# Kernel optimization log

Hardware: AMD Instinct MI355X
Metric: run time of the kernel (lower is better)

## Reference

```python
import jax, jax.numpy as jnp
import numpy as np

# ---- fixed structuring elements (buffers, not trainable) ----
N_SCALES = 4
BASE = 2.0
ZERO_SCALE = 1.0
PAD_VAL = 10000.0

_scales = ZERO_SCALE ** 2 * np.power(BASE, np.arange(N_SCALES)) ** 2  # t_k = 4^k
_widths = [4 * int(np.ceil(np.sqrt(s))) for s in _scales]             # 4,8,16,32
SES = [jnp.asarray([(1.0 / (4.0 * t)) * x ** 2 for x in range(-w, w + 1)],
                   dtype=jnp.float32)
       for t, w in zip(_scales, _widths)]  # SE lengths 9,17,33,65 (all odd)


def _pool1d(im, se, c, axis, is_max):
    """Weighted sliding max/min along `axis` (separable morphological op).
    out[p] = max_j padded[p+j] - c*se[j]  (dilation) or min_j padded[p+j] + c*se[j]."""
    n = se.shape[0]
    w = n // 2  # n is odd -> symmetric pad, matches torch pad1==pad2
    pad_val = -PAD_VAL if is_max else PAD_VAL
    cfg = [(0, 0)] * im.ndim
    cfg[axis] = (w, w)
    padded = jnp.pad(im, cfg, constant_values=pad_val)
    L = im.shape[axis]

    def take(j):
        return jax.lax.dynamic_slice_in_dim(padded, j, L, axis)

    win = jax.vmap(take)(jnp.arange(n))          # [n, B, C, H, W]
    se_b = se.reshape((n,) + (1,) * im.ndim)     # broadcast over image dims
    if is_max:
        return jnp.max(win - c * se_b, axis=0)
    return jnp.min(win + c * se_b, axis=0)


def _sep_dilation(im, se, c):
    tmp = _pool1d(im, se, c, axis=-1, is_max=True)   # horizontal
    return _pool1d(tmp, se, c, axis=-2, is_max=True)  # vertical


def _sep_erosion(im, se, c):
    tmp = _pool1d(im, se, c, axis=-1, is_max=False)
    return _pool1d(tmp, se, c, axis=-2, is_max=False)


def setup_inputs() -> dict:
    key = jax.random.key(0)
    k1, _ = jax.random.split(key)
    inputs = jax.random.normal(k1, (4, 8, 256, 256), dtype=jnp.float32)
    se_coef = jnp.float32(0.5)
    return {"inputs": inputs, "se_coef": se_coef}


def reference(inputs, se_coef):
    # closing = erosion(dilation(x)) per scale, stacked on new axis 2
    outs = [_sep_erosion(_sep_dilation(inputs, se, se_coef), se, se_coef)
            for se in SES]
    return jnp.stack(outs, axis=2)  # [B, C, n_scales, H, W]
```

## Files before the change

kernel.cpp:

```cpp
#include <hip/hip_runtime.h>


#define HH 256
#define WW 256
#define BC 32
#define NS 4
#define HW (HH * WW)
#define SLICE ((long)BC * HW)
#define LSTR 324

template <int W, bool IS_MAX>
__device__ __forceinline__ void hpass_lds(const float* __restrict__ lw, float cw,
                                          float acc[8])
{
    const float PAD = IS_MAX ? -1e30f : 1e30f;
#pragma unroll
    for (int pp = 0; pp < 8; ++pp) acc[pp] = PAD;
#pragma unroll
    for (int u = 0; u < (8 + 2 * W) / 4; ++u) {
        const float4 vv = *(const float4*)(lw + 4 * u);
        const float vs[4] = {vv.x, vv.y, vv.z, vv.w};
#pragma unroll
        for (int pp = 0; pp < 8; ++pp) {
#pragma unroll
            for (int e = 0; e < 4; ++e) {
                const int d = 4 * u + e - W - pp;
                if (d >= -W && d <= W) {
                    const float K = (float)(d * d);
                    const float cand = IS_MAX ? fmaf(cw, -K, vs[e])
                                              : fmaf(cw,  K, vs[e]);
                    acc[pp] = IS_MAX ? fmaxf(acc[pp], cand) : fminf(acc[pp], cand);
                }
            }
        }
    }
}

template <int W, bool IS_MAX, bool CLAMP>
__device__ __forceinline__ void vpass_core(const float* __restrict__ img, int x,
                                           int h0, float cw, float acc[8])
{
    const float PAD = IS_MAX ? -1e30f : 1e30f;
#pragma unroll
    for (int pp = 0; pp < 8; ++pp) acc[pp] = PAD;
#pragma unroll
    for (int ch = 0; ch < (8 + 2 * W) / 8; ++ch) {
        float v[8];
#pragma unroll
        for (int q = 0; q < 8; ++q) {
            const int h = h0 + ch * 8 + q - W;
            if (CLAMP) {
                const int hc = min(max(h, 0), HH - 1);
                const float tv = img[(long)hc * WW + x];
                v[q] = (h == hc) ? tv : PAD;
            } else {
                v[q] = img[(long)h * WW + x];
            }
        }
#pragma unroll
        for (int pp = 0; pp < 8; ++pp) {
#pragma unroll
            for (int q = 0; q < 8; ++q) {
                const int d = ch * 8 + q - W - pp;
                if (d >= -W && d <= W) {
                    const float K = (float)(d * d);
                    const float cand = IS_MAX ? fmaf(cw, -K, v[q])
                                              : fmaf(cw,  K, v[q]);
                    acc[pp] = IS_MAX ? fmaxf(acc[pp], cand) : fminf(acc[pp], cand);
                }
            }
        }
    }
}

template <int W, bool IS_MAX>
__device__ __forceinline__ void vh_tile(const float* __restrict__ img,
                                        float* __restrict__ op_base,
                                        int h0, float cw, float* lbuf)
{
    const int x = threadIdx.x;
    const float PAD = IS_MAX ? -1e30f : 1e30f;

    float vacc[8];
    if (h0 >= W && h0 + 8 + W <= HH)
        vpass_core<W, IS_MAX, false>(img, x, h0, cw, vacc);
    else
        vpass_core<W, IS_MAX, true >(img, x, h0, cw, vacc);

#pragma unroll
    for (int q = 0; q < 8; ++q) lbuf[q * LSTR + W + x] = vacc[q];
    if (x < W) {
#pragma unroll
        for (int q = 0; q < 8; ++q) {
            lbuf[q * LSTR + x] = PAD;
            lbuf[q * LSTR + W + 256 + x] = PAD;
        }
    }
    __syncthreads();

    const int r = threadIdx.x >> 5, t = threadIdx.x & 31;
    float acc[8];
    hpass_lds<W, IS_MAX>(lbuf + r * LSTR + 8 * t, cw, acc);
    float* op = op_base + (long)(h0 + r) * WW + 8 * t;
    *(float4*)(op)     = make_float4(acc[0], acc[1], acc[2], acc[3]);
    *(float4*)(op + 4) = make_float4(acc[4], acc[5], acc[6], acc[7]);

    __syncthreads();
}

template <int W, bool IS_MAX, int NT>
__device__ __forceinline__ void run_tiles(const float* __restrict__ ip,
                                          float* __restrict__ op,
                                          int y0, float c, float* lbuf)
{
    const float cw = c * (4.0f / (float)(W * W));
#pragma unroll 1
    for (int i = 0; i < NT; ++i)
        vh_tile<W, IS_MAX>(ip, op, (y0 + i) * 8, cw, lbuf);
}

template <bool IS_MAX>
__global__ __launch_bounds__(256, 8) void k_vh(const float* __restrict__ in,
                                               float* __restrict__ out,
                                               const float* __restrict__ cptr,
                                               long in_ks, long in_zs,
                                               long out_ks, long out_zs,
                                               int kfix, int bpz, int zbase)
{
    __shared__ float lbuf[8 * LSTR];
    const int bid = blockIdx.x;
    int k, y0, z;
    if (kfix < 0) {
        z = bid / 60;
        const int r = bid - z * 60;
        if (r < 32)      { k = 3; y0 = r; }
        else if (r < 48) { k = 2; y0 = (r - 32) * 2; }
        else if (r < 56) { k = 1; y0 = (r - 48) * 4; }
        else             { k = 0; y0 = (r - 56) * 8; }
    } else {
        k = kfix;
        const int zi = bid / bpz;
        const int yi = bid - zi * bpz;
        z = zbase + zi;
        y0 = yi * (32 / bpz);
    }
    const float c = cptr[0];
    const float* ip = in + (long)k * in_ks + (long)z * in_zs;
    float* op = out + (long)k * out_ks + (long)z * out_zs;
    switch (k) {
        case 0: run_tiles<4,  IS_MAX, 8>(ip, op, y0, c, lbuf); break;
        case 1: run_tiles<8,  IS_MAX, 4>(ip, op, y0, c, lbuf); break;
        case 2: run_tiles<16, IS_MAX, 2>(ip, op, y0, c, lbuf); break;
        case 3: run_tiles<32, IS_MAX, 1>(ip, op, y0, c, lbuf); break;
    }
}

extern "C" void kernel_launch(void* const* d_in, const int* in_sizes, int n_in,
                              void* d_out, int out_size, void* d_ws, size_t ws_size,
                              hipStream_t stream)
{
    const float* x = (const float*)d_in[0];
    const float* c = (const float*)d_in[1];
    float* out = (float*)d_out;
    float* ws  = (float*)d_ws;

    dim3 b(256);
    const size_t slice_b = (size_t)SLICE * sizeof(float);
    if (ws_size >= (size_t)NS * slice_b) {
        dim3 g(60 * BC);
        k_vh<true ><<<g, b, 0, stream>>>(x,  ws,  c, 0,     HW, SLICE, HW,
                                         -1, 0, 0);
        k_vh<false><<<g, b, 0, stream>>>(ws, out, c, SLICE, HW, HW, (long)NS * HW,
                                         -1, 0, 0);
    } else if (ws_size >= slice_b) {
        for (int k = 0; k < NS; ++k) {
            const int bpz = 4 << k;
            dim3 g(bpz * BC);
            k_vh<true ><<<g, b, 0, stream>>>(x,  ws,  c, 0, HW, 0, HW,
                                             k, bpz, 0);
            k_vh<false><<<g, b, 0, stream>>>(ws, out, c, 0, HW, HW, (long)NS * HW,
                                             k, bpz, 0);
        }
    } else {
        for (int k = 0; k < NS; ++k) {
            const int bpz = 4 << k;
            dim3 g(bpz);
            for (int z = 0; z < BC; ++z) {
                k_vh<true ><<<g, b, 0, stream>>>(x,  ws,  c, 0, HW, 0, 0,
                                                 k, bpz, z);
                k_vh<false><<<g, b, 0, stream>>>(ws, out, c, 0, 0, HW, (long)NS * HW,
                                                 k, bpz, z);
            }
        }
    }
}
```

Baseline: 119.7 us.

## Double-buffer LDS tiles to drop trailing barrier and pair max/min ops

Inlines the tile loop into run_tiles and alternates between two LDS buffers per tile, which removes the second __syncthreads per tile. The LDS row stride now depends on the window width, and small windows load the whole vertical column window at once. The inner max/min loops handle two taps per step with a nested fmax/fmin. The cost is double the LDS footprint and more register pressure from the larger unrolled loads for W<=8.

```diff
diff --git a/kernel.cpp b/kernel.cpp
--- a/kernel.cpp
+++ b/kernel.cpp
@@ -7,7 +7,9 @@
 #define NS 4
 #define HW (HH * WW)
 #define SLICE ((long)BC * HW)
-#define LSTR 324
+
+template <int W> struct LdsStride { static constexpr int v = 2 * W + 256 + 4; };
+#define LBUF_FLOATS (2 * 8 * 292)
 
 template <int W, bool IS_MAX>
 __device__ __forceinline__ void hpass_lds(const float* __restrict__ lw, float cw,
@@ -23,13 +25,28 @@
 #pragma unroll
         for (int pp = 0; pp < 8; ++pp) {
 #pragma unroll
-            for (int e = 0; e < 4; ++e) {
-                const int d = 4 * u + e - W - pp;
-                if (d >= -W && d <= W) {
-                    const float K = (float)(d * d);
-                    const float cand = IS_MAX ? fmaf(cw, -K, vs[e])
-                                              : fmaf(cw,  K, vs[e]);
-                    acc[pp] = IS_MAX ? fmaxf(acc[pp], cand) : fminf(acc[pp], cand);
+            for (int e = 0; e < 4; e += 2) {
+                const int d1 = 4 * u + e - W - pp;
+                const int d2 = d1 + 1;
+                const bool ok1 = (d1 >= -W) && (d1 <= W);
+                const bool ok2 = (d2 >= -W) && (d2 <= W);
+                const float K1 = (float)(d1 * d1);
+                const float K2 = (float)(d2 * d2);
+                if (ok1 && ok2) {
+                    const float c1 = IS_MAX ? fmaf(cw, -K1, vs[e])
+                                            : fmaf(cw,  K1, vs[e]);
+                    const float c2 = IS_MAX ? fmaf(cw, -K2, vs[e + 1])
+                                            : fmaf(cw,  K2, vs[e + 1]);
+                    acc[pp] = IS_MAX ? fmaxf(acc[pp], fmaxf(c1, c2))
+                                     : fminf(acc[pp], fminf(c1, c2));
+                } else if (ok1) {
+                    const float c1 = IS_MAX ? fmaf(cw, -K1, vs[e])
+                                            : fmaf(cw,  K1, vs[e]);
+                    acc[pp] = IS_MAX ? fmaxf(acc[pp], c1) : fminf(acc[pp], c1);
+                } else if (ok2) {
+                    const float c2 = IS_MAX ? fmaf(cw, -K2, vs[e + 1])
+                                            : fmaf(cw,  K2, vs[e + 1]);
+                    acc[pp] = IS_MAX ? fmaxf(acc[pp], c2) : fminf(acc[pp], c2);
                 }
             }
         }
@@ -41,14 +58,16 @@
                                            int h0, float cw, float acc[8])
 {
     const float PAD = IS_MAX ? -1e30f : 1e30f;
+    constexpr int TOT = 8 + 2 * W;
+    constexpr int CH = (W <= 8) ? TOT : 8;
 #pragma unroll
     for (int pp = 0; pp < 8; ++pp) acc[pp] = PAD;
 #pragma unroll
-    for (int ch = 0; ch < (8 + 2 * W) / 8; ++ch) {
-        float v[8];
-#pragma unroll
-        for (int q = 0; q < 8; ++q) {
-            const int h = h0 + ch * 8 + q - W;
+    for (int ch = 0; ch < TOT / CH; ++ch) {
+        float v[CH];
+#pragma unroll
+        for (int q = 0; q < CH; ++q) {
+            const int h = h0 + ch * CH + q - W;
             if (CLAMP) {
                 const int hc = min(max(h, 0), HH - 1);
                 const float tv = img[(long)hc * WW + x];
@@ -60,52 +79,32 @@
 #pragma unroll
         for (int pp = 0; pp < 8; ++pp) {
 #pragma unroll
-            for (int q = 0; q < 8; ++q) {
-                const int d = ch * 8 + q - W - pp;
-                if (d >= -W && d <= W) {
-                    const float K = (float)(d * d);
-                    const float cand = IS_MAX ? fmaf(cw, -K, v[q])
-                                              : fmaf(cw,  K, v[q]);
-                    acc[pp] = IS_MAX ? fmaxf(acc[pp], cand) : fminf(acc[pp], cand);
+            for (int q = 0; q < CH; q += 2) {
+                const int d1 = ch * CH + q - W - pp;
+                const int d2 = d1 + 1;
+                const bool ok1 = (d1 >= -W) && (d1 <= W);
+                const bool ok2 = (d2 >= -W) && (d2 <= W);
+                const float K1 = (float)(d1 * d1);
+                const float K2 = (float)(d2 * d2);
+                if (ok1 && ok2) {
+                    const float c1 = IS_MAX ? fmaf(cw, -K1, v[q])
+                                            : fmaf(cw,  K1, v[q]);
+                    const float c2 = IS_MAX ? fmaf(cw, -K2, v[q + 1])
+                                            : fmaf(cw,  K2, v[q + 1]);
+                    acc[pp] = IS_MAX ? fmaxf(acc[pp], fmaxf(c1, c2))
+                                     : fminf(acc[pp], fminf(c1, c2));
+                } else if (ok1) {
+                    const float c1 = IS_MAX ? fmaf(cw, -K1, v[q])
+                                            : fmaf(cw,  K1, v[q]);
+                    acc[pp] = IS_MAX ? fmaxf(acc[pp], c1) : fminf(acc[pp], c1);
+                } else if (ok2) {
+                    const float c2 = IS_MAX ? fmaf(cw, -K2, v[q + 1])
+                                            : fmaf(cw,  K2, v[q + 1]);
+                    acc[pp] = IS_MAX ? fmaxf(acc[pp], c2) : fminf(acc[pp], c2);
                 }
             }
         }
     }
-}
-
-template <int W, bool IS_MAX>
-__device__ __forceinline__ void vh_tile(const float* __restrict__ img,
-                                        float* __restrict__ op_base,
-                                        int h0, float cw, float* lbuf)
-{
-    const int x = threadIdx.x;
-    const float PAD = IS_MAX ? -1e30f : 1e30f;
-
-    float vacc[8];
-    if (h0 >= W && h0 + 8 + W <= HH)
-        vpass_core<W, IS_MAX, false>(img, x, h0, cw, vacc);
-    else
-        vpass_core<W, IS_MAX, true >(img, x, h0, cw, vacc);
-
-#pragma unroll
-    for (int q = 0; q < 8; ++q) lbuf[q * LSTR + W + x] = vacc[q];
-    if (x < W) {
-#pragma unroll
-        for (int q = 0; q < 8; ++q) {
-            lbuf[q * LSTR + x] = PAD;
-            lbuf[q * LSTR + W + 256 + x] = PAD;
-        }
-    }
-    __syncthreads();
-
-    const int r = threadIdx.x >> 5, t = threadIdx.x & 31;
-    float acc[8];
-    hpass_lds<W, IS_MAX>(lbuf + r * LSTR + 8 * t, cw, acc);
-    float* op = op_base + (long)(h0 + r) * WW + 8 * t;
-    *(float4*)(op)     = make_float4(acc[0], acc[1], acc[2], acc[3]);
-    *(float4*)(op + 4) = make_float4(acc[4], acc[5], acc[6], acc[7]);
-
-    __syncthreads();
 }
 
 template <int W, bool IS_MAX, int NT>
@@ -113,10 +112,40 @@
                                           float* __restrict__ op,
                                           int y0, float c, float* lbuf)
 {
+    constexpr int LS = LdsStride<W>::v;
     const float cw = c * (4.0f / (float)(W * W));
+    const float PAD = IS_MAX ? -1e30f : 1e30f;
+    const int x = threadIdx.x;
+    const int r = threadIdx.x >> 5, t = threadIdx.x & 31;
+
 #pragma unroll 1
-    for (int i = 0; i < NT; ++i)
-        vh_tile<W, IS_MAX>(ip, op, (y0 + i) * 8, cw, lbuf);
+    for (int i = 0; i < NT; ++i) {
+        float* buf = lbuf + (i & 1) * 8 * LS;
+        const int h0 = (y0 + i) * 8;
+
+        float vacc[8];
+        if (h0 >= W && h0 + 8 + W <= HH)
+            vpass_core<W, IS_MAX, false>(ip, x, h0, cw, vacc);
+        else
+            vpass_core<W, IS_MAX, true >(ip, x, h0, cw, vacc);
+
+#pragma unroll
+        for (int q = 0; q < 8; ++q) buf[q * LS + W + x] = vacc[q];
+        if (x < W) {
+#pragma unroll
+            for (int q = 0; q < 8; ++q) {
+                buf[q * LS + x] = PAD;
+                buf[q * LS + W + 256 + x] = PAD;
+            }
+        }
+        __syncthreads();
+
+        float acc[8];
+        hpass_lds<W, IS_MAX>(buf + r * LS + 8 * t, cw, acc);
+        float* o = op + (long)(h0 + r) * WW + 8 * t;
+        *(float4*)(o)     = make_float4(acc[0], acc[1], acc[2], acc[3]);
+        *(float4*)(o + 4) = make_float4(acc[4], acc[5], acc[6], acc[7]);
+    }
 }
 
 template <bool IS_MAX>
@@ -127,7 +156,7 @@
                                                long out_ks, long out_zs,
                                                int kfix, int bpz, int zbase)
 {
-    __shared__ float lbuf[8 * LSTR];
+    __shared__ __align__(16) float lbuf[LBUF_FLOATS];
     const int bid = blockIdx.x;
     int k, y0, z;
     if (kfix < 0) {
```

Measured after the change: 128.6 us. +7.5%, slower.
